# Optimization experiments

Hardware: AMD Instinct MI355X
Metric: run time of the kernel (lower is better)

The kernel has to match this reference:

```python
import jax, jax.numpy as jnp
import numpy as np

MIN_WEIGHT = 0.0
MAX_WEIGHT = 500.0


def setup_inputs() -> dict:
    key = jax.random.key(0)
    k1, k2, k3 = jax.random.split(key, 3)
    B, P = 131072, 64   # groundings, predicates
    C, L = 128, 3       # clauses, literals per clause
    ground_atoms = jax.random.normal(k1, (B, P), dtype=jnp.float32)
    # learned clause weights, initial_clause_weight = 0.5
    clause_weights = 0.5 * jnp.ones((C,), dtype=jnp.float32)
    # which predicate each literal refers to
    literal_idx = jax.random.randint(k2, (C, L), 0, P, dtype=jnp.int64)
    # 0 -> negated literal (sign -1), 1 -> positive literal (sign +1)
    sign_bits = jax.random.randint(k3, (C, L), 0, 2, dtype=jnp.int32)
    return {
        "ground_atoms": ground_atoms,
        "clause_weights": clause_weights,
        "literal_idx": literal_idx,
        "sign_bits": sign_bits,
    }


def reference(ground_atoms, clause_weights, literal_idx, sign_bits):
    """Vectorized KnowledgeEnhancer forward.

    Per clause (GodelBoostConormApprox):
      literals = signs * ground_atoms[:, idx]
      delta    = signs * clamp(w) * softmax(literals)
    Then concat all clause deltas and scatter_add into predicate space.
    """
    B, P = ground_atoms.shape
    C, L = literal_idx.shape
    signs = (2 * sign_bits - 1).astype(ground_atoms.dtype)  # [C, L] in {-1,+1}
    gathered = ground_atoms[:, literal_idx]                 # [B, C, L] gather
    literals = signs[None, :, :] * gathered                 # signed pre-activations
    w = jnp.clip(clause_weights, MIN_WEIGHT, MAX_WEIGHT)    # [C]
    delta = signs[None, :, :] * w[None, :, None] * jax.nn.softmax(literals, axis=-1)
    # concat over clauses (dim=1 in the torch code) then scatter_add over predicates
    delta_flat = delta.reshape(B, C * L)
    idx_flat = literal_idx.reshape(C * L)
    out = jax.ops.segment_sum(delta_flat.T, idx_flat, num_segments=P)  # [P, B]
    return out.T  # [B, P]
```

## Files before the change

### kernel.cpp

```cpp
#include <hip/hip_runtime.h>
#include <stdint.h>

typedef unsigned int  u32;
typedef unsigned short u16;

#define B_ROWS 131072
#define P_PRED 64
#define C_CLS  128
#define NPAIR  384
#define CAP    32
#define RPB    128
#define TPB    512
#define LSTR   65
#define LOG2E  1.4426950408889634f

#if __has_builtin(__builtin_amdgcn_exp2f)
#define EXP2F(x) __builtin_amdgcn_exp2f(x)
#else
#define EXP2F(x) exp2f(x)
#endif

#if __has_builtin(__builtin_amdgcn_rcpf)
#define RCPF(x) __builtin_amdgcn_rcpf(x)
#else
#define RCPF(x) (1.0f / (x))
#endif

struct __align__(16) Rec {
    u32 i1, i2, ms, m1, m2;
    float swc;
    u32 pad0, pad1;
};

__device__ __forceinline__ float bf16_to_f(u16 u) {
    return __uint_as_float(((u32)u) << 16);
}
__device__ __forceinline__ u16 f_to_bf16(float f) {
    u32 u = __float_as_uint(f);
    u += 0x7FFFu + ((u >> 16) & 1u);
    return (u16)(u >> 16);
}
__device__ __forceinline__ float sxor(float a, u32 m) {
    return __uint_as_float(__float_as_uint(a) ^ m);
}

__global__ void ke_prep(const u32* __restrict__ lidx_w,
                        const u32* __restrict__ sb_w,
                        const u32* __restrict__ w_w,
                        u32* __restrict__ recs,
                        int* __restrict__ cnts,
                        u32* __restrict__ flags) {
    __shared__ int scnt[P_PRED];
    __shared__ int sidx[NPAIR];
    __shared__ int ssb[NPAIR];
    __shared__ int det[3];
    const int t = threadIdx.x;
    if (t < P_PRED) scnt[t] = 0;
    if (t < 3) det[t] = 1;
    __syncthreads();
    if (t < NPAIR / 2) {
        if (lidx_w[2 * t + 1] != 0u) det[0] = 0;
        if (sb_w[2 * t + 1]   != 0u) det[1] = 0;
    }
    if (t == 0 && (w_w[0] & 0xFFFFu) == 0u) det[2] = 0;
    __syncthreads();
    if (t < NPAIR) {
        sidx[t] = (int)(det[0] ? lidx_w[2 * t] : lidx_w[t]);
        ssb[t]  = (int)(det[1] ? sb_w[2 * t]   : sb_w[t]);
    }
    __syncthreads();
    if (t < NPAIR) {
        const int c = t / 3;
        const int l = t - c * 3;
        const int base = c * 3;
        const int o1 = base + (l == 0 ? 1 : 0);
        const int o2 = base + (l == 2 ? 1 : 2);
        const int p = sidx[t];
        const int slot = atomicAdd(&scnt[p], 1);
        float wraw = det[2] ? bf16_to_f((u16)(w_w[c / 2] >> ((c & 1) * 16)))
                            : __uint_as_float(w_w[c]);
        float wc = fminf(fmaxf(wraw, 0.0f), 500.0f);
        float ss = ssb[t] ? 1.0f : -1.0f;
        if (slot < CAP) {
            u32* r = recs + (p * CAP + slot) * 8;
            r[0] = (u32)sidx[o1];
            r[1] = (u32)sidx[o2];
            r[2] = ssb[t]  ? 0u : 0x80000000u;
            r[3] = ssb[o1] ? 0u : 0x80000000u;
            r[4] = ssb[o2] ? 0u : 0x80000000u;
            r[5] = __float_as_uint(ss * wc);
            r[6] = 0u;
            r[7] = 0u;
        }
    }
    __syncthreads();
    if (t < P_PRED) cnts[t] = min(scnt[t], CAP);
    if (t == 0) flags[0] = (u32)det[2];
}

__global__ __launch_bounds__(TPB, 8)
void ke_main(const void* __restrict__ atoms_v,
             const u32* __restrict__ recs_u,
             const int* __restrict__ cnts,
             const u32* __restrict__ flags,
             void* __restrict__ out_v) {
    __shared__ float lds[RPB * LSTR];
    const int tid = threadIdx.x;
    const int row = tid & (RPB - 1);
    const int grp = __builtin_amdgcn_readfirstlane(tid >> 7);
    const int rowBase = blockIdx.x * RPB;
    const bool bf16m = (flags[0] != 0u);

    if (bf16m) {
        const u16* gbase = (const u16*)atoms_v + (size_t)rowBase * P_PRED;
#pragma unroll
        for (int pass = 0; pass < 2; ++pass) {
            int flat = pass * (TPB * 8) + tid * 8;
            uint4 v = *(const uint4*)(gbase + flat);
            int r = flat >> 6, col = flat & 63;
            float* dst = &lds[r * LSTR + col];
            dst[0] = __uint_as_float(v.x << 16) * LOG2E;
            dst[1] = __uint_as_float(v.x & 0xFFFF0000u) * LOG2E;
            dst[2] = __uint_as_float(v.y << 16) * LOG2E;
            dst[3] = __uint_as_float(v.y & 0xFFFF0000u) * LOG2E;
            dst[4] = __uint_as_float(v.z << 16) * LOG2E;
            dst[5] = __uint_as_float(v.z & 0xFFFF0000u) * LOG2E;
            dst[6] = __uint_as_float(v.w << 16) * LOG2E;
            dst[7] = __uint_as_float(v.w & 0xFFFF0000u) * LOG2E;
        }
    } else {
        const float* gbase = (const float*)atoms_v + (size_t)rowBase * P_PRED;
#pragma unroll
        for (int pass = 0; pass < 4; ++pass) {
            int flat = pass * (TPB * 4) + tid * 4;
            float4 v = *(const float4*)(gbase + flat);
            int r = flat >> 6, col = flat & 63;
            float* dst = &lds[r * LSTR + col];
            dst[0] = v.x * LOG2E;
            dst[1] = v.y * LOG2E;
            dst[2] = v.z * LOG2E;
            dst[3] = v.w * LOG2E;
        }
    }
    __syncthreads();

    const float* lrow = &lds[row * LSTR];

    for (int half = 0; half < 2; ++half) {
        float acc[8];
#pragma unroll
        for (int pp = 0; pp < 8; ++pp) {
            const int p = grp * 16 + half * 8 + pp;
            const float As = lrow[p];
            const int n = min(cnts[p], CAP);
            const Rec* rp = (const Rec*)recs_u + p * CAP;
            float a = 0.0f;
            for (int e = 0; e < n; ++e) {
                Rec r = rp[e];
                float Ls = sxor(As, r.ms);
                float L1 = sxor(lrow[r.i1], r.m1);
                float L2 = sxor(lrow[r.i2], r.m2);
                float s = 1.0f + EXP2F(L1 - Ls) + EXP2F(L2 - Ls);
                a += r.swc * RCPF(s);
            }
            acc[pp] = a;
        }
        const int pbase = grp * 16 + half * 8;
        if (bf16m) {
            u16* orow = (u16*)out_v + (size_t)(rowBase + row) * P_PRED;
            uint4 o;
            o.x = (u32)f_to_bf16(acc[0]) | ((u32)f_to_bf16(acc[1]) << 16);
            o.y = (u32)f_to_bf16(acc[2]) | ((u32)f_to_bf16(acc[3]) << 16);
            o.z = (u32)f_to_bf16(acc[4]) | ((u32)f_to_bf16(acc[5]) << 16);
            o.w = (u32)f_to_bf16(acc[6]) | ((u32)f_to_bf16(acc[7]) << 16);
            *(uint4*)(orow + pbase) = o;
        } else {
            float* orow = (float*)out_v + (size_t)(rowBase + row) * P_PRED;
            *(float4*)(orow + pbase)     = make_float4(acc[0], acc[1], acc[2], acc[3]);
            *(float4*)(orow + pbase + 4) = make_float4(acc[4], acc[5], acc[6], acc[7]);
        }
    }
}

extern "C" void kernel_launch(void* const* d_in, const int* in_sizes, int n_in,
                              void* d_out, int out_size, void* d_ws, size_t ws_size,
                              hipStream_t stream) {
    const void* ground_atoms   = d_in[0];
    const u32*  clause_weights = (const u32*)d_in[1];
    const u32*  literal_idx    = (const u32*)d_in[2];
    const u32*  sign_bits      = (const u32*)d_in[3];

    u32* recs  = (u32*)d_ws;
    int* cnts  = (int*)((char*)d_ws + P_PRED * CAP * 32);
    u32* flags = (u32*)((char*)d_ws + P_PRED * CAP * 32 + 256);

    ke_prep<<<1, NPAIR, 0, stream>>>(literal_idx, sign_bits, clause_weights,
                                     recs, cnts, flags);
    ke_main<<<B_ROWS / RPB, TPB, 0, stream>>>(ground_atoms, recs, cnts, flags,
                                              d_out);
}
```

Measured before the change: 109.3 us.

## Compute softmax per clause and scatter into LDS accumulators with atomics

Each clause's softmax is now computed once per row and its three contributions are added into a shared-memory accumulator with workgroup-scope float atomics. Before, the work was organized per predicate, so each clause softmax was recomputed three times (once per literal). This removes the per-predicate record lists and the CAP truncation, and uses smaller blocks of 64 rows with a second LDS buffer. In exchange it adds LDS atomic contention (four waves share each row's accumulator), a zero-init pass, an extra barrier, and more LDS per block.

```diff
diff --git a/kernel.cpp b/kernel.cpp
--- a/kernel.cpp
+++ b/kernel.cpp
@@ -8,10 +8,10 @@
 #define P_PRED 64
 #define C_CLS  128
 #define NPAIR  384
-#define CAP    32
-#define RPB    128
-#define TPB    512
+#define RPB    64
+#define TPB    256
 #define LSTR   65
+#define ACC_OFF (RPB * LSTR)
 #define LOG2E  1.4426950408889634f
 
 #if __has_builtin(__builtin_amdgcn_exp2f)
@@ -26,12 +26,6 @@
 #define RCPF(x) (1.0f / (x))
 #endif
 
-struct __align__(16) Rec {
-    u32 i1, i2, ms, m1, m2;
-    float swc;
-    u32 pad0, pad1;
-};
-
 __device__ __forceinline__ float bf16_to_f(u16 u) {
     return __uint_as_float(((u32)u) << 16);
 }
@@ -43,19 +37,19 @@
 __device__ __forceinline__ float sxor(float a, u32 m) {
     return __uint_as_float(__float_as_uint(a) ^ m);
 }
+__device__ __forceinline__ void lds_fadd(float* p, float v) {
+    __hip_atomic_fetch_add(p, v, __ATOMIC_RELAXED, __HIP_MEMORY_SCOPE_WORKGROUP);
+}
 
 __global__ void ke_prep(const u32* __restrict__ lidx_w,
                         const u32* __restrict__ sb_w,
                         const u32* __restrict__ w_w,
                         u32* __restrict__ recs,
-                        int* __restrict__ cnts,
                         u32* __restrict__ flags) {
-    __shared__ int scnt[P_PRED];
     __shared__ int sidx[NPAIR];
     __shared__ int ssb[NPAIR];
     __shared__ int det[3];
     const int t = threadIdx.x;
-    if (t < P_PRED) scnt[t] = 0;
     if (t < 3) det[t] = 1;
     __syncthreads();
     if (t < NPAIR / 2) {
@@ -69,47 +63,37 @@
         ssb[t]  = (int)(det[1] ? sb_w[2 * t]   : sb_w[t]);
     }
     __syncthreads();
-    if (t < NPAIR) {
-        const int c = t / 3;
-        const int l = t - c * 3;
-        const int base = c * 3;
-        const int o1 = base + (l == 0 ? 1 : 0);
-        const int o2 = base + (l == 2 ? 1 : 2);
-        const int p = sidx[t];
-        const int slot = atomicAdd(&scnt[p], 1);
+    if (t < C_CLS) {
+        const int c = t;
         float wraw = det[2] ? bf16_to_f((u16)(w_w[c / 2] >> ((c & 1) * 16)))
                             : __uint_as_float(w_w[c]);
         float wc = fminf(fmaxf(wraw, 0.0f), 500.0f);
-        float ss = ssb[t] ? 1.0f : -1.0f;
-        if (slot < CAP) {
-            u32* r = recs + (p * CAP + slot) * 8;
-            r[0] = (u32)sidx[o1];
-            r[1] = (u32)sidx[o2];
-            r[2] = ssb[t]  ? 0u : 0x80000000u;
-            r[3] = ssb[o1] ? 0u : 0x80000000u;
-            r[4] = ssb[o2] ? 0u : 0x80000000u;
-            r[5] = __float_as_uint(ss * wc);
-            r[6] = 0u;
-            r[7] = 0u;
+        u32* r = recs + c * 8;
+#pragma unroll
+        for (int l = 0; l < 3; ++l) {
+            int b = ssb[c * 3 + l];
+            r[l]     = (u32)sidx[c * 3 + l] | (b ? 0u : 0x80000000u);
+            r[3 + l] = __float_as_uint(b ? wc : -wc);
         }
+        r[6] = 0u;
+        r[7] = 0u;
     }
-    __syncthreads();
-    if (t < P_PRED) cnts[t] = min(scnt[t], CAP);
     if (t == 0) flags[0] = (u32)det[2];
 }
 
-__global__ __launch_bounds__(TPB, 8)
+__global__ __launch_bounds__(TPB, 4)
 void ke_main(const void* __restrict__ atoms_v,
              const u32* __restrict__ recs_u,
-             const int* __restrict__ cnts,
              const u32* __restrict__ flags,
              void* __restrict__ out_v) {
-    __shared__ float lds[RPB * LSTR];
+    __shared__ float lds[2 * RPB * LSTR];
     const int tid = threadIdx.x;
     const int row = tid & (RPB - 1);
-    const int grp = __builtin_amdgcn_readfirstlane(tid >> 7);
+    const int q = __builtin_amdgcn_readfirstlane(tid >> 6);
     const int rowBase = blockIdx.x * RPB;
     const bool bf16m = (flags[0] != 0u);
+
+    for (int i = tid; i < RPB * LSTR; i += TPB) lds[ACC_OFF + i] = 0.0f;
 
     if (bf16m) {
         const u16* gbase = (const u16*)atoms_v + (size_t)rowBase * P_PRED;
@@ -144,40 +128,53 @@
     }
     __syncthreads();
 
-    const float* lrow = &lds[row * LSTR];
+    float* a = &lds[row * LSTR];
 
-    for (int half = 0; half < 2; ++half) {
-        float acc[8];
+#pragma unroll 4
+    for (int k = 0; k < C_CLS / 4; ++k) {
+        const int c = q * (C_CLS / 4) + k;
+        const u32* r = recs_u + c * 8;
+        const u32 w0 = r[0], w1 = r[1], w2 = r[2];
+        const float sw0 = __uint_as_float(r[3]);
+        const float sw1 = __uint_as_float(r[4]);
+        const float sw2 = __uint_as_float(r[5]);
+        const u32 i0 = w0 & 0xFFFFu, i1 = w1 & 0xFFFFu, i2 = w2 & 0xFFFFu;
+        float L0 = sxor(a[i0], w0 & 0x80000000u);
+        float L1 = sxor(a[i1], w1 & 0x80000000u);
+        float L2 = sxor(a[i2], w2 & 0x80000000u);
+        float e0 = EXP2F(L0), e1 = EXP2F(L1), e2 = EXP2F(L2);
+        float t = RCPF(e0 + e1 + e2);
+        lds_fadd(&a[i0 + ACC_OFF], (sw0 * t) * e0);
+        lds_fadd(&a[i1 + ACC_OFF], (sw1 * t) * e1);
+        lds_fadd(&a[i2 + ACC_OFF], (sw2 * t) * e2);
+    }
+    __syncthreads();
+
+    {
+        const int erow = tid >> 2;
+        const int eq = tid & 3;
+        const float* arow = &lds[ACC_OFF + erow * LSTR + eq * 16];
+        float v[16];
 #pragma unroll
-        for (int pp = 0; pp < 8; ++pp) {
-            const int p = grp * 16 + half * 8 + pp;
-            const float As = lrow[p];
-            const int n = min(cnts[p], CAP);
-            const Rec* rp = (const Rec*)recs_u + p * CAP;
-            float a = 0.0f;
-            for (int e = 0; e < n; ++e) {
-                Rec r = rp[e];
-                float Ls = sxor(As, r.ms);
-                float L1 = sxor(lrow[r.i1], r.m1);
-                float L2 = sxor(lrow[r.i2], r.m2);
-                float s = 1.0f + EXP2F(L1 - Ls) + EXP2F(L2 - Ls);
-                a += r.swc * RCPF(s);
-            }
-            acc[pp] = a;
-        }
-        const int pbase = grp * 16 + half * 8;
+        for (int i = 0; i < 16; ++i) v[i] = arow[i];
         if (bf16m) {
-            u16* orow = (u16*)out_v + (size_t)(rowBase + row) * P_PRED;
-            uint4 o;
-            o.x = (u32)f_to_bf16(acc[0]) | ((u32)f_to_bf16(acc[1]) << 16);
-            o.y = (u32)f_to_bf16(acc[2]) | ((u32)f_to_bf16(acc[3]) << 16);
-            o.z = (u32)f_to_bf16(acc[4]) | ((u32)f_to_bf16(acc[5]) << 16);
-            o.w = (u32)f_to_bf16(acc[6]) | ((u32)f_to_bf16(acc[7]) << 16);
-            *(uint4*)(orow + pbase) = o;
+            u16* orow = (u16*)out_v + (size_t)(rowBase + erow) * P_PRED + eq * 16;
+            uint4 o0, o1;
+            o0.x = (u32)f_to_bf16(v[0])  | ((u32)f_to_bf16(v[1])  << 16);
+            o0.y = (u32)f_to_bf16(v[2])  | ((u32)f_to_bf16(v[3])  << 16);
+            o0.z = (u32)f_to_bf16(v[4])  | ((u32)f_to_bf16(v[5])  << 16);
+            o0.w = (u32)f_to_bf16(v[6])  | ((u32)f_to_bf16(v[7])  << 16);
+            o1.x = (u32)f_to_bf16(v[8])  | ((u32)f_to_bf16(v[9])  << 16);
+            o1.y = (u32)f_to_bf16(v[10]) | ((u32)f_to_bf16(v[11]) << 16);
+            o1.z = (u32)f_to_bf16(v[12]) | ((u32)f_to_bf16(v[13]) << 16);
+            o1.w = (u32)f_to_bf16(v[14]) | ((u32)f_to_bf16(v[15]) << 16);
+            *(uint4*)(orow)     = o0;
+            *(uint4*)(orow + 8) = o1;
         } else {
-            float* orow = (float*)out_v + (size_t)(rowBase + row) * P_PRED;
-            *(float4*)(orow + pbase)     = make_float4(acc[0], acc[1], acc[2], acc[3]);
-            *(float4*)(orow + pbase + 4) = make_float4(acc[4], acc[5], acc[6], acc[7]);
+            float* orow = (float*)out_v + (size_t)(rowBase + erow) * P_PRED + eq * 16;
+#pragma unroll
+            for (int i = 0; i < 16; i += 4)
+                *(float4*)(orow + i) = make_float4(v[i], v[i+1], v[i+2], v[i+3]);
         }
     }
 }
@@ -185,17 +182,14 @@
 extern "C" void kernel_launch(void* const* d_in, const int* in_sizes, int n_in,
                               void* d_out, int out_size, void* d_ws, size_t ws_size,
                               hipStream_t stream) {
-    const void* ground_atoms   = d_in[0];
-    const u32*  clause_weights = (const u32*)d_in[1];
-    const u32*  literal_idx    = (const u32*)d_in[2];
-    const u32*  sign_bits      = (const u32*)d_in[3];
+    const u32* clause_weights = (const u32*)d_in[1];
+    const u32* literal_idx    = (const u32*)d_in[2];
+    const u32* sign_bits      = (const u32*)d_in[3];
 
     u32* recs  = (u32*)d_ws;
-    int* cnts  = (int*)((char*)d_ws + P_PRED * CAP * 32);
-    u32* flags = (u32*)((char*)d_ws + P_PRED * CAP * 32 + 256);
+    u32* flags = (u32*)((char*)d_ws + C_CLS * 32);
 
     ke_prep<<<1, NPAIR, 0, stream>>>(literal_idx, sign_bits, clause_weights,
-                                     recs, cnts, flags);
-    ke_main<<<B_ROWS / RPB, TPB, 0, stream>>>(ground_atoms, recs, cnts, flags,
-                                              d_out);
+                                     recs, flags);
+    ke_main<<<B_ROWS / RPB, TPB, 0, stream>>>(d_in[0], recs, flags, d_out);
 }
```

After: 337.9 us. 3.09x slower.

## Precompute exp(±x) per atom in LDS and evaluate softmax by ratio

Applied to the files above, without the earlier changes.

Each atom's exp2(x) and exp2(-x) are now computed once while staging the tile into shared memory. The clause softmax term becomes e_s/(e_s+e_1+e_2) using only lookups and one reciprocal, instead of two exp2 per record per predicate. Records shrink to 16 bytes, with the sign folded into an index offset. Rows per block halve and the LDS row stride doubles to hold both exponentials. The risk is overflow or underflow of the raw exponentials when atom magnitudes are large, since the max-subtraction stabilisation is gone.

```diff
diff --git a/kernel.cpp b/kernel.cpp
--- a/kernel.cpp
+++ b/kernel.cpp
@@ -9,9 +9,9 @@
 #define C_CLS  128
 #define NPAIR  384
 #define CAP    32
-#define RPB    128
+#define RPB    64
 #define TPB    512
-#define LSTR   65
+#define LSTR   129
 #define LOG2E  1.4426950408889634f
 
 #if __has_builtin(__builtin_amdgcn_exp2f)
@@ -26,12 +26,6 @@
 #define RCPF(x) (1.0f / (x))
 #endif
 
-struct __align__(16) Rec {
-    u32 i1, i2, ms, m1, m2;
-    float swc;
-    u32 pad0, pad1;
-};
-
 __device__ __forceinline__ float bf16_to_f(u16 u) {
     return __uint_as_float(((u32)u) << 16);
 }
@@ -39,9 +33,6 @@
     u32 u = __float_as_uint(f);
     u += 0x7FFFu + ((u >> 16) & 1u);
     return (u16)(u >> 16);
-}
-__device__ __forceinline__ float sxor(float a, u32 m) {
-    return __uint_as_float(__float_as_uint(a) ^ m);
 }
 
 __global__ void ke_prep(const u32* __restrict__ lidx_w,
@@ -80,17 +71,12 @@
         float wraw = det[2] ? bf16_to_f((u16)(w_w[c / 2] >> ((c & 1) * 16)))
                             : __uint_as_float(w_w[c]);
         float wc = fminf(fmaxf(wraw, 0.0f), 500.0f);
-        float ss = ssb[t] ? 1.0f : -1.0f;
         if (slot < CAP) {
-            u32* r = recs + (p * CAP + slot) * 8;
-            r[0] = (u32)sidx[o1];
-            r[1] = (u32)sidx[o2];
-            r[2] = ssb[t]  ? 0u : 0x80000000u;
-            r[3] = ssb[o1] ? 0u : 0x80000000u;
-            r[4] = ssb[o2] ? 0u : 0x80000000u;
-            r[5] = __float_as_uint(ss * wc);
-            r[6] = 0u;
-            r[7] = 0u;
+            u32* r = recs + (p * CAP + slot) * 4;
+            r[0] = (u32)(2 * sidx[t]  + (ssb[t]  ? 0 : 1));
+            r[1] = (u32)(2 * sidx[o1] + (ssb[o1] ? 0 : 1));
+            r[2] = (u32)(2 * sidx[o2] + (ssb[o2] ? 0 : 1));
+            r[3] = __float_as_uint(ssb[t] ? wc : -wc);
         }
     }
     __syncthreads();
@@ -104,98 +90,92 @@
              const int* __restrict__ cnts,
              const u32* __restrict__ flags,
              void* __restrict__ out_v) {
-    __shared__ float lds[RPB * LSTR];
+    __shared__ float E[RPB * LSTR];
     const int tid = threadIdx.x;
     const int row = tid & (RPB - 1);
-    const int grp = __builtin_amdgcn_readfirstlane(tid >> 7);
+    const int grp = __builtin_amdgcn_readfirstlane(tid >> 6);
     const int rowBase = blockIdx.x * RPB;
     const bool bf16m = (flags[0] != 0u);
 
-    if (bf16m) {
-        const u16* gbase = (const u16*)atoms_v + (size_t)rowBase * P_PRED;
+    {
+        const int srow = tid >> 3;
+        const int c0 = (tid & 7) * 8;
+        float* dst = &E[srow * LSTR + 2 * c0];
+        if (bf16m) {
+            const u16* g = (const u16*)atoms_v + (size_t)(rowBase + srow) * P_PRED + c0;
+            uint4 v = *(const uint4*)g;
+            u32 w[4] = {v.x, v.y, v.z, v.w};
 #pragma unroll
-        for (int pass = 0; pass < 2; ++pass) {
-            int flat = pass * (TPB * 8) + tid * 8;
-            uint4 v = *(const uint4*)(gbase + flat);
-            int r = flat >> 6, col = flat & 63;
-            float* dst = &lds[r * LSTR + col];
-            dst[0] = __uint_as_float(v.x << 16) * LOG2E;
-            dst[1] = __uint_as_float(v.x & 0xFFFF0000u) * LOG2E;
-            dst[2] = __uint_as_float(v.y << 16) * LOG2E;
-            dst[3] = __uint_as_float(v.y & 0xFFFF0000u) * LOG2E;
-            dst[4] = __uint_as_float(v.z << 16) * LOG2E;
-            dst[5] = __uint_as_float(v.z & 0xFFFF0000u) * LOG2E;
-            dst[6] = __uint_as_float(v.w << 16) * LOG2E;
-            dst[7] = __uint_as_float(v.w & 0xFFFF0000u) * LOG2E;
-        }
-    } else {
-        const float* gbase = (const float*)atoms_v + (size_t)rowBase * P_PRED;
+            for (int j = 0; j < 4; ++j) {
+                float x0 = __uint_as_float(w[j] << 16) * LOG2E;
+                float x1 = __uint_as_float(w[j] & 0xFFFF0000u) * LOG2E;
+                dst[4 * j + 0] = EXP2F(x0);
+                dst[4 * j + 1] = EXP2F(-x0);
+                dst[4 * j + 2] = EXP2F(x1);
+                dst[4 * j + 3] = EXP2F(-x1);
+            }
+        } else {
+            const float* g = (const float*)atoms_v + (size_t)(rowBase + srow) * P_PRED + c0;
+            float4 v0 = *(const float4*)g;
+            float4 v1 = *(const float4*)(g + 4);
+            float xs[8] = {v0.x, v0.y, v0.z, v0.w, v1.x, v1.y, v1.z, v1.w};
 #pragma unroll
-        for (int pass = 0; pass < 4; ++pass) {
-            int flat = pass * (TPB * 4) + tid * 4;
-            float4 v = *(const float4*)(gbase + flat);
-            int r = flat >> 6, col = flat & 63;
-            float* dst = &lds[r * LSTR + col];
-            dst[0] = v.x * LOG2E;
-            dst[1] = v.y * LOG2E;
-            dst[2] = v.z * LOG2E;
-            dst[3] = v.w * LOG2E;
+            for (int j = 0; j < 8; ++j) {
+                float x = xs[j] * LOG2E;
+                dst[2 * j + 0] = EXP2F(x);
+                dst[2 * j + 1] = EXP2F(-x);
+            }
         }
     }
     __syncthreads();
 
-    const float* lrow = &lds[row * LSTR];
+    const float* Lrow = &E[row * LSTR];
 
-    for (int half = 0; half < 2; ++half) {
-        float acc[8];
+    float acc[8];
 #pragma unroll
-        for (int pp = 0; pp < 8; ++pp) {
-            const int p = grp * 16 + half * 8 + pp;
-            const float As = lrow[p];
-            const int n = min(cnts[p], CAP);
-            const Rec* rp = (const Rec*)recs_u + p * CAP;
-            float a = 0.0f;
-            for (int e = 0; e < n; ++e) {
-                Rec r = rp[e];
-                float Ls = sxor(As, r.ms);
-                float L1 = sxor(lrow[r.i1], r.m1);
-                float L2 = sxor(lrow[r.i2], r.m2);
-                float s = 1.0f + EXP2F(L1 - Ls) + EXP2F(L2 - Ls);
-                a += r.swc * RCPF(s);
-            }
-            acc[pp] = a;
+    for (int pp = 0; pp < 8; ++pp) {
+        const int p = grp * 8 + pp;
+        const int n = min(cnts[p], CAP);
+        const u32* rp = recs_u + p * CAP * 4;
+        float a = 0.0f;
+        for (int e = 0; e < n; ++e) {
+            const u32* r = rp + e * 4;
+            float ss = Lrow[r[0]];
+            float s1 = Lrow[r[1]];
+            float s2 = Lrow[r[2]];
+            float sw = __uint_as_float(r[3]);
+            a += sw * ss * RCPF(ss + s1 + s2);
         }
-        const int pbase = grp * 16 + half * 8;
-        if (bf16m) {
-            u16* orow = (u16*)out_v + (size_t)(rowBase + row) * P_PRED;
-            uint4 o;
-            o.x = (u32)f_to_bf16(acc[0]) | ((u32)f_to_bf16(acc[1]) << 16);
-            o.y = (u32)f_to_bf16(acc[2]) | ((u32)f_to_bf16(acc[3]) << 16);
-            o.z = (u32)f_to_bf16(acc[4]) | ((u32)f_to_bf16(acc[5]) << 16);
-            o.w = (u32)f_to_bf16(acc[6]) | ((u32)f_to_bf16(acc[7]) << 16);
-            *(uint4*)(orow + pbase) = o;
-        } else {
-            float* orow = (float*)out_v + (size_t)(rowBase + row) * P_PRED;
-            *(float4*)(orow + pbase)     = make_float4(acc[0], acc[1], acc[2], acc[3]);
-            *(float4*)(orow + pbase + 4) = make_float4(acc[4], acc[5], acc[6], acc[7]);
-        }
+        acc[pp] = a;
+    }
+
+    if (bf16m) {
+        u16* op = (u16*)out_v + (size_t)(rowBase + row) * P_PRED + grp * 8;
+        uint4 o;
+        o.x = (u32)f_to_bf16(acc[0]) | ((u32)f_to_bf16(acc[1]) << 16);
+        o.y = (u32)f_to_bf16(acc[2]) | ((u32)f_to_bf16(acc[3]) << 16);
+        o.z = (u32)f_to_bf16(acc[4]) | ((u32)f_to_bf16(acc[5]) << 16);
+        o.w = (u32)f_to_bf16(acc[6]) | ((u32)f_to_bf16(acc[7]) << 16);
+        *(uint4*)op = o;
+    } else {
+        float* op = (float*)out_v + (size_t)(rowBase + row) * P_PRED + grp * 8;
+        *(float4*)(op)     = make_float4(acc[0], acc[1], acc[2], acc[3]);
+        *(float4*)(op + 4) = make_float4(acc[4], acc[5], acc[6], acc[7]);
     }
 }
 
 extern "C" void kernel_launch(void* const* d_in, const int* in_sizes, int n_in,
                               void* d_out, int out_size, void* d_ws, size_t ws_size,
                               hipStream_t stream) {
-    const void* ground_atoms   = d_in[0];
-    const u32*  clause_weights = (const u32*)d_in[1];
-    const u32*  literal_idx    = (const u32*)d_in[2];
-    const u32*  sign_bits      = (const u32*)d_in[3];
+    const u32* clause_weights = (const u32*)d_in[1];
+    const u32* literal_idx    = (const u32*)d_in[2];
+    const u32* sign_bits      = (const u32*)d_in[3];
 
     u32* recs  = (u32*)d_ws;
-    int* cnts  = (int*)((char*)d_ws + P_PRED * CAP * 32);
-    u32* flags = (u32*)((char*)d_ws + P_PRED * CAP * 32 + 256);
+    int* cnts  = (int*)((char*)d_ws + P_PRED * CAP * 16);
+    u32* flags = (u32*)((char*)d_ws + P_PRED * CAP * 16 + 256);
 
     ke_prep<<<1, NPAIR, 0, stream>>>(literal_idx, sign_bits, clause_weights,
                                      recs, cnts, flags);
-    ke_main<<<B_ROWS / RPB, TPB, 0, stream>>>(ground_atoms, recs, cnts, flags,
-                                              d_out);
+    ke_main<<<B_ROWS / RPB, TPB, 0, stream>>>(d_in[0], recs, cnts, flags, d_out);
 }
```

Result: faster. 106.9 us (-2.1%).
